# Performance work log

Measured on AMD Instinct MI355X. Metric: run time of the kernel, lower is better.

## Reference

```python
import jax, jax.numpy as jnp
import numpy as np
from jax import lax

ALPHA = 2.0
EROSIONS = 10


def setup_inputs() -> dict:
    key = jax.random.key(0)
    k1, k2 = jax.random.split(key)
    B, C, H, W = 32, 1, 1024, 1024
    pred = jax.random.uniform(k1, (B, C, H, W), dtype=jnp.float32)
    target = jax.random.uniform(k2, (B, C, H, W), dtype=jnp.float32)
    return {"pred": pred, "target": target}


def _hausdorff_er_loss(pred, target):
    # 3x3 cross structuring element * 0.2 (sums to 1), as in kernel2D
    kernel = jnp.array([[0.0, 0.2, 0.0],
                        [0.2, 0.2, 0.2],
                        [0.0, 0.2, 0.0]], dtype=pred.dtype)
    kernel = kernel[None, None]  # OIHW: (1,1,3,3)

    bound = (pred - target) ** 2  # (B,1,H,W)

    def step(carry, k):
        b, acc = carry
        # scipy.ndimage.convolve(mode='constant', cval=0) == SAME zero-padded conv;
        # the cross kernel is symmetric so correlation == convolution.
        dil = lax.conv_general_dilated(
            b, kernel, window_strides=(1, 1), padding='SAME',
            dimension_numbers=('NCHW', 'OIHW', 'NCHW'))
        er = jnp.maximum(dil - 0.5, 0.0)
        # per-sample min/max normalization (ptp over the whole (1,H,W) array)
        emin = er.min(axis=(1, 2, 3), keepdims=True)
        emax = er.max(axis=(1, 2, 3), keepdims=True)
        ptp = emax - emin
        er = jnp.where(ptp > 0, (er - emin) / jnp.where(ptp > 0, ptp, 1.0), er)
        acc = acc + er * (k + 1.0) ** ALPHA
        return (er, acc), None

    ks = jnp.arange(EROSIONS, dtype=bound.dtype)
    (_, eroted), _ = lax.scan(step, (bound, jnp.zeros_like(bound)), ks)
    return eroted.mean()


def reference(pred, target):
    return _hausdorff_er_loss(pred, target)
```

## Files before the change

kernel.cpp:

```cpp
#include <hip/hip_runtime.h>

#define BATCH 32
#define HH 1024
#define WW 1024
#define NPIX (HH * WW)
#define NEROS 10
#define TPS 64
#define NTILES (BATCH * TPS)
#define FWPS 32

__device__ __forceinline__ float4 ld4f(const float* p) {
    return *reinterpret_cast<const float4*>(p);
}

__global__ __launch_bounds__(512, 4) void conv0_kernel(
    const float* __restrict__ pred, const float* __restrict__ tgt,
    float* __restrict__ out, unsigned* __restrict__ Fout,
    unsigned* __restrict__ cntOut, unsigned* __restrict__ omin,
    unsigned* __restrict__ omax, double* __restrict__ osum) {
    int blk = blockIdx.x;
    blk = (blk & 7) * (NTILES >> 3) + (blk >> 3);
    const int s = blk >> 6, ty = blk & 63, ry = ty << 4;
    const int tid = threadIdx.x, lane = tid & 63, w = tid >> 6;
    const size_t sbase = (size_t)s * NPIX;

    __shared__ float sb[18 * 1024];

    float4 pv[9], tv[9];
#pragma unroll
    for (int i = 0; i < 9; ++i) {
        const int slot = tid + 512 * i;
        const int y = ry - 1 + (slot >> 8);
        if (y >= 0 && y < HH) {
            const size_t idx = sbase + (size_t)y * WW + ((slot & 255) << 2);
            pv[i] = ld4f(pred + idx);
            tv[i] = ld4f(tgt + idx);
        } else {
            pv[i] = make_float4(0.f, 0.f, 0.f, 0.f);
            tv[i] = make_float4(0.f, 0.f, 0.f, 0.f);
        }
    }
#pragma unroll
    for (int i = 0; i < 9; ++i) {
        const int slot = tid + 512 * i;
        float4 b;
        b.x = (pv[i].x - tv[i].x) * (pv[i].x - tv[i].x);
        b.y = (pv[i].y - tv[i].y) * (pv[i].y - tv[i].y);
        b.z = (pv[i].z - tv[i].z) * (pv[i].z - tv[i].z);
        b.w = (pv[i].w - tv[i].w) * (pv[i].w - tv[i].w);
        *reinterpret_cast<float4*>(
            &sb[(slot >> 8) * 1024 + ((slot & 255) << 2)]) = b;
    }
    __syncthreads();

    float lmin = 3.4e38f, lmax = 0.f, lsum = 0.f;
    unsigned rowbits = 0u;
#pragma unroll
    for (int rr = 0; rr < 2; ++rr) {
        const int yl = (w << 1) + rr;
        const int y = ry + yl;
        float O[16];
        bool nz = false;
#pragma unroll
        for (int q = 0; q < 4; ++q) {
            const int xw = (q << 8) + (lane << 2);
            const float4 U = *(const float4*)&sb[yl * 1024 + xw];
            const float4 Cc = *(const float4*)&sb[(yl + 1) * 1024 + xw];
            const float4 D = *(const float4*)&sb[(yl + 2) * 1024 + xw];
            float lf = __shfl_up(Cc.w, 1);
            if (lane == 0)
                lf = (q > 0) ? sb[(yl + 1) * 1024 + (q << 8) - 1] : 0.f;
            float rt = __shfl_down(Cc.x, 1);
            if (lane == 63)
                rt = (q < 3) ? sb[(yl + 1) * 1024 + (q << 8) + 256] : 0.f;
            const float cv[4] = {Cc.x, Cc.y, Cc.z, Cc.w};
            const float uv[4] = {U.x, U.y, U.z, U.w};
            const float dv[4] = {D.x, D.y, D.z, D.w};
            const float lvv[4] = {lf, Cc.x, Cc.y, Cc.z};
            const float rvv[4] = {Cc.y, Cc.z, Cc.w, rt};
#pragma unroll
            for (int j = 0; j < 4; ++j) {
                const float conv =
                    0.2f * (uv[j] + dv[j] + cv[j] + lvv[j] + rvv[j]);
                const float er = fmaxf(conv - 0.5f, 0.f);
                O[(q << 2) + j] = er;
                lmin = fminf(lmin, er);
                lmax = fmaxf(lmax, er);
                lsum += er;
                nz = nz || (er > 0.f);
            }
        }
        if (__ballot(nz) != 0ull) {
            const size_t ob = sbase + (size_t)y * WW;
#pragma unroll
            for (int q = 0; q < 4; ++q)
                *reinterpret_cast<float4*>(out + ob + (q << 8) + (lane << 2)) =
                    make_float4(O[q << 2], O[(q << 2) + 1], O[(q << 2) + 2],
                                O[(q << 2) + 3]);
            rowbits |= 1u << yl;
        }
    }

#pragma unroll
    for (int off = 32; off > 0; off >>= 1) {
        lmin = fminf(lmin, __shfl_down(lmin, off));
        lmax = fmaxf(lmax, __shfl_down(lmax, off));
        lsum += __shfl_down(lsum, off);
    }
    __shared__ float smn[8], smx[8], ssm[8];
    __shared__ unsigned sfb[8];
    if (lane == 0) {
        smn[w] = lmin;
        smx[w] = lmax;
        ssm[w] = lsum;
        sfb[w] = rowbits;
    }
    __syncthreads();
    if (tid == 0) {
        unsigned fmask = 0u;
        float bmn = smn[0], bmx = smx[0], bsm = ssm[0];
        fmask = sfb[0];
#pragma unroll
        for (int i = 1; i < 8; ++i) {
            bmn = fminf(bmn, smn[i]);
            bmx = fmaxf(bmx, smx[i]);
            bsm += ssm[i];
            fmask |= sfb[i];
        }
        if (fmask) {
            atomicOr(&Fout[s * FWPS + (ty >> 1)], fmask << ((ty & 1) * 16));
            atomicAdd(cntOut, 1u);
        }
        atomicMin(&omin[s], __float_as_uint(bmn));
        if (bmx > 0.f) atomicMax(&omax[s], __float_as_uint(bmx));
        if (bsm > 0.f) atomicAdd(&osum[s], (double)bsm);
    }
}

__global__ __launch_bounds__(256, 4) void convt_kernel(
    const float* __restrict__ in, float* __restrict__ out,
    const unsigned* __restrict__ Fprev, unsigned* __restrict__ Fout,
    const unsigned* __restrict__ cntPrev, unsigned* __restrict__ cntOut,
    const unsigned* __restrict__ pmin, const unsigned* __restrict__ pmax,
    unsigned* __restrict__ omin, unsigned* __restrict__ omax,
    double* __restrict__ osum) {
    if (*cntPrev == 0u) return;

    int blk = blockIdx.x;
    blk = (blk & 7) * (NTILES >> 3) + (blk >> 3);
    const int s = blk >> 6, ty = blk & 63, ry = ty << 4;
    const int tid = threadIdx.x, lane = tid & 63, w = tid >> 6;
    const int xb = lane << 4;
    const size_t sbase = (size_t)s * NPIX;

    const unsigned* Fs = Fprev + s * FWPS;
    const int w32 = ty >> 1, sh = (ty & 1) * 16;
    const unsigned cur = Fs[w32];
    unsigned M = ((cur >> sh) & 0xFFFFu) << 1;
    if (ty > 0)
        M |= (ty & 1) ? ((cur >> 15) & 1u) : ((Fs[w32 - 1] >> 31) & 1u);
    if (ty < TPS - 1) {
        const unsigned nb = (ty & 1) ? (Fs[w32 + 1] & 1u) : ((cur >> 16) & 1u);
        M |= nb << 17;
    }
    if (M == 0u) {
        if (tid == 0) atomicMin(&omin[s], 0u);
        return;
    }

    float a = 1.f, cc = 0.f;
    {
        const float mn = __uint_as_float(pmin[s]);
        const float mx = __uint_as_float(pmax[s]);
        const float ptp = mx - mn;
        if (ptp > 0.f) { a = 1.f / ptp; cc = mn; }
    }

    const int r0 = w << 2;
    float A[16], B[16], C[16], O[16];

    auto loadRow = [&](int y, float* V) {
        const bool ok =
            (y >= 0 && y < HH) && (((M >> (y - ry + 1)) & 1u) != 0u);
        if (!ok) {
#pragma unroll
            for (int j = 0; j < 16; ++j) V[j] = 0.f;
            return;
        }
        const size_t idx = sbase + (size_t)y * WW + xb;
#pragma unroll
        for (int q = 0; q < 4; ++q) {
            const float4 v = ld4f(in + idx + 4 * q);
            V[4 * q + 0] = v.x;
            V[4 * q + 1] = v.y;
            V[4 * q + 2] = v.z;
            V[4 * q + 3] = v.w;
        }
    };

    loadRow(ry + r0 - 1, A);
    loadRow(ry + r0, B);

    float lmin = 3.4e38f, lmax = 0.f, lsum = 0.f;
    unsigned rowbits = 0u;

#pragma unroll
    for (int r = 0; r < 4; ++r) {
        const int y = ry + r0 + r;
        loadRow(y + 1, C);
        const bool act = (((M >> (r0 + r)) & 7u) != 0u);
        if (act) {
            float lfe = __shfl_up(B[15], 1);
            if (lane == 0) lfe = 0.f;
            float rte = __shfl_down(B[0], 1);
            if (lane == 63) rte = 0.f;
            const float vert =
                1.f + (y > 0 ? 1.f : 0.f) + (y < HH - 1 ? 1.f : 0.f);
            bool nz = false;
#pragma unroll
            for (int j = 0; j < 16; ++j) {
                const float lf = (j == 0) ? lfe : B[j - 1];
                const float rt = (j == 15) ? rte : B[j + 1];
                const float conv = 0.2f * (A[j] + C[j] + B[j] + lf + rt);
                const int x = xb + j;
                const float kf = 0.2f * (vert + (x > 0 ? 1.f : 0.f) +
                                         (x < WW - 1 ? 1.f : 0.f));
                const float dil = (conv - cc * kf) * a;
                const float er = fmaxf(dil - 0.5f, 0.f);
                O[j] = er;
                lmin = fminf(lmin, er);
                lmax = fmaxf(lmax, er);
                lsum += er;
                nz = nz || (er > 0.f);
            }
            if (__ballot(nz) != 0ull) {
                const size_t oidx = sbase + (size_t)y * WW + xb;
#pragma unroll
                for (int q = 0; q < 4; ++q)
                    *reinterpret_cast<float4*>(out + oidx + 4 * q) =
                        make_float4(O[4 * q], O[4 * q + 1], O[4 * q + 2],
                                    O[4 * q + 3]);
                rowbits |= 1u << (r0 + r);
            }
        } else {
            lmin = fminf(lmin, 0.f);
        }
#pragma unroll
        for (int j = 0; j < 16; ++j) {
            A[j] = B[j];
            B[j] = C[j];
        }
    }

#pragma unroll
    for (int off = 32; off > 0; off >>= 1) {
        lmin = fminf(lmin, __shfl_down(lmin, off));
        lmax = fmaxf(lmax, __shfl_down(lmax, off));
        lsum += __shfl_down(lsum, off);
    }
    __shared__ float smn[4], smx[4], ssm[4];
    __shared__ unsigned sfb[4];
    if (lane == 0) {
        smn[w] = lmin;
        smx[w] = lmax;
        ssm[w] = lsum;
        sfb[w] = rowbits;
    }
    __syncthreads();
    if (tid == 0) {
        const unsigned fmask = sfb[0] | sfb[1] | sfb[2] | sfb[3];
        float bmn = smn[0], bmx = smx[0], bsm = ssm[0];
#pragma unroll
        for (int i = 1; i < 4; ++i) {
            bmn = fminf(bmn, smn[i]);
            bmx = fmaxf(bmx, smx[i]);
            bsm += ssm[i];
        }
        if (fmask) {
            atomicOr(&Fout[s * FWPS + w32], fmask << sh);
            atomicAdd(cntOut, 1u);
        }
        atomicMin(&omin[s], __float_as_uint(bmn));
        if (bmx > 0.f) atomicMax(&omax[s], __float_as_uint(bmx));
        if (bsm > 0.f) atomicAdd(&osum[s], (double)bsm);
    }
}

__global__ void init_kernel(unsigned* __restrict__ minb,
                            unsigned* __restrict__ maxb,
                            double* __restrict__ sums,
                            unsigned* __restrict__ F,
                            unsigned* __restrict__ cnt) {
    const int i = blockIdx.x * blockDim.x + threadIdx.x;
    if (i < NEROS * BATCH) {
        minb[i] = 0x7f800000u;
        maxb[i] = 0u;
        sums[i] = 0.0;
    }
    if (i < NEROS * BATCH * FWPS) F[i] = 0u;
    if (i < NEROS) cnt[i] = 0u;
}

__global__ void final_kernel(const unsigned* __restrict__ minb,
                             const unsigned* __restrict__ maxb,
                             const double* __restrict__ sums,
                             float* __restrict__ out) {
    const int s = threadIdx.x;
    double tot = 0.0;
    if (s < BATCH) {
        for (int k = 0; k < NEROS; ++k) {
            const float mn = __uint_as_float(minb[k * BATCH + s]);
            const float mx = __uint_as_float(maxb[k * BATCH + s]);
            const double sm = sums[k * BATCH + s];
            const float ptp = mx - mn;
            double v;
            if (ptp > 0.f)
                v = (sm - (double)NPIX * (double)mn) / (double)ptp;
            else
                v = sm;
            tot += (double)((k + 1) * (k + 1)) * v;
        }
    }
#pragma unroll
    for (int off = 32; off > 0; off >>= 1) tot += __shfl_down(tot, off);
    if (s == 0) out[0] = (float)(tot / ((double)BATCH * (double)NPIX));
}

extern "C" void kernel_launch(void* const* d_in, const int* in_sizes, int n_in,
                              void* d_out, int out_size, void* d_ws,
                              size_t ws_size, hipStream_t stream) {
    const float* pred = (const float*)d_in[0];
    const float* tgt = (const float*)d_in[1];
    float* out = (float*)d_out;

    float* buf0 = (float*)d_ws;
    float* buf1 = buf0 + (size_t)BATCH * NPIX;
    unsigned* minb = (unsigned*)(buf1 + (size_t)BATCH * NPIX);
    unsigned* maxb = minb + NEROS * BATCH;
    double* sums = (double*)(maxb + NEROS * BATCH);
    unsigned* F = (unsigned*)(sums + NEROS * BATCH);
    unsigned* cnt = F + (size_t)NEROS * BATCH * FWPS;

    init_kernel<<<40, 256, 0, stream>>>(minb, maxb, sums, F, cnt);

    conv0_kernel<<<NTILES, 512, 0, stream>>>(pred, tgt, buf0, F, &cnt[0], minb,
                                             maxb, sums);

    float* bufs[2] = {buf0, buf1};
    for (int k = 1; k < NEROS; ++k) {
        const float* src = bufs[(k - 1) & 1];
        float* dst = bufs[k & 1];
        convt_kernel<<<NTILES, 256, 0, stream>>>(
            src, dst, F + (size_t)(k - 1) * BATCH * FWPS,
            F + (size_t)k * BATCH * FWPS, &cnt[k - 1], &cnt[k],
            minb + (size_t)(k - 1) * BATCH, maxb + (size_t)(k - 1) * BATCH,
            minb + (size_t)k * BATCH, maxb + (size_t)k * BATCH,
            sums + (size_t)k * BATCH);
    }

    final_kernel<<<1, 64, 0, stream>>>(minb, maxb, sums, out);
}
```

Measured before the change: 131.3 us.

## Restructure first erosion kernel to keep 8-row column strips in registers

The first convolution kernel now works on 8-row tiles with 256 threads. Each wave owns a 256-column strip, and the rows stay in registers instead of a 72KB shared-memory tile. Only the wave-seam column values go through shared memory, and row flags are set per wave with atomics. This removes the large shared allocation to improve occupancy and cut LDS traffic. In exchange, the vertical halo re-read grows from 2 of 18 rows to 2 of 10, and output rows are now always stored.

New measurement: 250.3 us. +90.6%, slower.

```diff
diff --git a/kernel.cpp b/kernel.cpp
--- a/kernel.cpp
+++ b/kernel.cpp
@@ -8,31 +8,34 @@
 #define TPS 64
 #define NTILES (BATCH * TPS)
 #define FWPS 32
+#define NB0 (BATCH * 128)
 
 __device__ __forceinline__ float4 ld4f(const float* p) {
     return *reinterpret_cast<const float4*>(p);
 }
 
-__global__ __launch_bounds__(512, 4) void conv0_kernel(
+__global__ __launch_bounds__(256, 4) void conv0_kernel(
     const float* __restrict__ pred, const float* __restrict__ tgt,
     float* __restrict__ out, unsigned* __restrict__ Fout,
     unsigned* __restrict__ cntOut, unsigned* __restrict__ omin,
     unsigned* __restrict__ omax, double* __restrict__ osum) {
     int blk = blockIdx.x;
-    blk = (blk & 7) * (NTILES >> 3) + (blk >> 3);
-    const int s = blk >> 6, ty = blk & 63, ry = ty << 4;
+    blk = (blk & 7) * (NB0 >> 3) + (blk >> 3);
+    const int s = blk >> 7, g = blk & 127;
+    const int y0 = g << 3;
     const int tid = threadIdx.x, lane = tid & 63, w = tid >> 6;
     const size_t sbase = (size_t)s * NPIX;
-
-    __shared__ float sb[18 * 1024];
-
-    float4 pv[9], tv[9];
-#pragma unroll
-    for (int i = 0; i < 9; ++i) {
-        const int slot = tid + 512 * i;
-        const int y = ry - 1 + (slot >> 8);
+    const int xb = (w << 8) + (lane << 2);
+
+    __shared__ float seamL[4][8], seamR[4][8];
+    __shared__ float smn[4], smx[4], ssm[4];
+
+    float4 pv[10], tv[10];
+#pragma unroll
+    for (int i = 0; i < 10; ++i) {
+        const int y = y0 - 1 + i;
         if (y >= 0 && y < HH) {
-            const size_t idx = sbase + (size_t)y * WW + ((slot & 255) << 2);
+            const size_t idx = sbase + (size_t)y * WW + xb;
             pv[i] = ld4f(pred + idx);
             tv[i] = ld4f(tgt + idx);
         } else {
@@ -40,65 +43,58 @@
             tv[i] = make_float4(0.f, 0.f, 0.f, 0.f);
         }
     }
-#pragma unroll
-    for (int i = 0; i < 9; ++i) {
-        const int slot = tid + 512 * i;
-        float4 b;
-        b.x = (pv[i].x - tv[i].x) * (pv[i].x - tv[i].x);
-        b.y = (pv[i].y - tv[i].y) * (pv[i].y - tv[i].y);
-        b.z = (pv[i].z - tv[i].z) * (pv[i].z - tv[i].z);
-        b.w = (pv[i].w - tv[i].w) * (pv[i].w - tv[i].w);
-        *reinterpret_cast<float4*>(
-            &sb[(slot >> 8) * 1024 + ((slot & 255) << 2)]) = b;
+
+    float b[10][4];
+#pragma unroll
+    for (int i = 0; i < 10; ++i) {
+        b[i][0] = (pv[i].x - tv[i].x) * (pv[i].x - tv[i].x);
+        b[i][1] = (pv[i].y - tv[i].y) * (pv[i].y - tv[i].y);
+        b[i][2] = (pv[i].z - tv[i].z) * (pv[i].z - tv[i].z);
+        b[i][3] = (pv[i].w - tv[i].w) * (pv[i].w - tv[i].w);
+    }
+
+    if (lane == 0) {
+#pragma unroll
+        for (int r = 1; r <= 8; ++r) seamL[w][r - 1] = b[r][0];
+    }
+    if (lane == 63) {
+#pragma unroll
+        for (int r = 1; r <= 8; ++r) seamR[w][r - 1] = b[r][3];
     }
     __syncthreads();
 
     float lmin = 3.4e38f, lmax = 0.f, lsum = 0.f;
     unsigned rowbits = 0u;
 #pragma unroll
-    for (int rr = 0; rr < 2; ++rr) {
-        const int yl = (w << 1) + rr;
-        const int y = ry + yl;
-        float O[16];
+    for (int r = 1; r <= 8; ++r) {
+        const int y = y0 + r - 1;
+        float lf0 = __shfl_up(b[r][3], 1);
+        if (lane == 0) lf0 = (w > 0) ? seamR[w - 1][r - 1] : 0.f;
+        float rt3 = __shfl_down(b[r][0], 1);
+        if (lane == 63) rt3 = (w < 3) ? seamL[w + 1][r - 1] : 0.f;
+        const float lv[4] = {lf0, b[r][0], b[r][1], b[r][2]};
+        const float rv[4] = {b[r][1], b[r][2], b[r][3], rt3};
+        float O[4];
         bool nz = false;
 #pragma unroll
-        for (int q = 0; q < 4; ++q) {
-            const int xw = (q << 8) + (lane << 2);
-            const float4 U = *(const float4*)&sb[yl * 1024 + xw];
-            const float4 Cc = *(const float4*)&sb[(yl + 1) * 1024 + xw];
-            const float4 D = *(const float4*)&sb[(yl + 2) * 1024 + xw];
-            float lf = __shfl_up(Cc.w, 1);
-            if (lane == 0)
-                lf = (q > 0) ? sb[(yl + 1) * 1024 + (q << 8) - 1] : 0.f;
-            float rt = __shfl_down(Cc.x, 1);
-            if (lane == 63)
-                rt = (q < 3) ? sb[(yl + 1) * 1024 + (q << 8) + 256] : 0.f;
-            const float cv[4] = {Cc.x, Cc.y, Cc.z, Cc.w};
-            const float uv[4] = {U.x, U.y, U.z, U.w};
-            const float dv[4] = {D.x, D.y, D.z, D.w};
-            const float lvv[4] = {lf, Cc.x, Cc.y, Cc.z};
-            const float rvv[4] = {Cc.y, Cc.z, Cc.w, rt};
-#pragma unroll
-            for (int j = 0; j < 4; ++j) {
-                const float conv =
-                    0.2f * (uv[j] + dv[j] + cv[j] + lvv[j] + rvv[j]);
-                const float er = fmaxf(conv - 0.5f, 0.f);
-                O[(q << 2) + j] = er;
-                lmin = fminf(lmin, er);
-                lmax = fmaxf(lmax, er);
-                lsum += er;
-                nz = nz || (er > 0.f);
-            }
-        }
-        if (__ballot(nz) != 0ull) {
-            const size_t ob = sbase + (size_t)y * WW;
-#pragma unroll
-            for (int q = 0; q < 4; ++q)
-                *reinterpret_cast<float4*>(out + ob + (q << 8) + (lane << 2)) =
-                    make_float4(O[q << 2], O[(q << 2) + 1], O[(q << 2) + 2],
-                                O[(q << 2) + 3]);
-            rowbits |= 1u << yl;
-        }
+        for (int j = 0; j < 4; ++j) {
+            const float conv =
+                0.2f * (b[r - 1][j] + b[r + 1][j] + b[r][j] + lv[j] + rv[j]);
+            const float er = fmaxf(conv - 0.5f, 0.f);
+            O[j] = er;
+            lmin = fminf(lmin, er);
+            lmax = fmaxf(lmax, er);
+            lsum += er;
+            nz = nz || (er > 0.f);
+        }
+        *reinterpret_cast<float4*>(out + sbase + (size_t)y * WW + xb) =
+            make_float4(O[0], O[1], O[2], O[3]);
+        if (__ballot(nz) != 0ull) rowbits |= 1u << (r - 1);
+    }
+
+    if (lane == 0 && rowbits) {
+        atomicOr(&Fout[s * FWPS + (g >> 2)], rowbits << ((g & 3) * 8));
+        atomicAdd(cntOut, 1u);
     }
 
 #pragma unroll
@@ -107,29 +103,19 @@
         lmax = fmaxf(lmax, __shfl_down(lmax, off));
         lsum += __shfl_down(lsum, off);
     }
-    __shared__ float smn[8], smx[8], ssm[8];
-    __shared__ unsigned sfb[8];
     if (lane == 0) {
         smn[w] = lmin;
         smx[w] = lmax;
         ssm[w] = lsum;
-        sfb[w] = rowbits;
     }
     __syncthreads();
     if (tid == 0) {
-        unsigned fmask = 0u;
         float bmn = smn[0], bmx = smx[0], bsm = ssm[0];
-        fmask = sfb[0];
-#pragma unroll
-        for (int i = 1; i < 8; ++i) {
+#pragma unroll
+        for (int i = 1; i < 4; ++i) {
             bmn = fminf(bmn, smn[i]);
             bmx = fmaxf(bmx, smx[i]);
             bsm += ssm[i];
-            fmask |= sfb[i];
-        }
-        if (fmask) {
-            atomicOr(&Fout[s * FWPS + (ty >> 1)], fmask << ((ty & 1) * 16));
-            atomicAdd(cntOut, 1u);
         }
         atomicMin(&omin[s], __float_as_uint(bmn));
         if (bmx > 0.f) atomicMax(&omax[s], __float_as_uint(bmx));
@@ -343,8 +329,8 @@
 
     init_kernel<<<40, 256, 0, stream>>>(minb, maxb, sums, F, cnt);
 
-    conv0_kernel<<<NTILES, 512, 0, stream>>>(pred, tgt, buf0, F, &cnt[0], minb,
-                                             maxb, sums);
+    conv0_kernel<<<NB0, 256, 0, stream>>>(pred, tgt, buf0, F, &cnt[0], minb,
+                                          maxb, sums);
 
     float* bufs[2] = {buf0, buf1};
     for (int k = 1; k < NEROS; ++k) {
```
